# Performance work log

Hardware: AMD Instinct MI355X
Metric: run time of the kernel (lower is better)

Reference implementation:

```python
import jax, jax.numpy as jnp
import numpy as np

NODE = 5
FML = 64                     # hidden_size // node_num = 320 // 5
F0, F1, FO = 256, 256, 256   # fc_numbers
D_IN = (FML + 1) * 2         # each node has in-degree 2 -> 130
# graph[i,j]==1 means edge i->j; parents of node i = sorted nonzero of column i
# graph = ring: graph[i][(i+1)%5] = graph[i][(i+2)%5] = 1
PARENTS = np.array([[3, 4], [0, 4], [0, 1], [1, 2], [2, 3]], dtype=np.int32)
BN_EPS = 1e-5


def setup_inputs() -> dict:
    key = jax.random.key(0)
    ks = jax.random.split(key, 14)
    B, T = 8192, 128
    s = 0.05
    f32 = jnp.float32
    return {
        "x":   jax.random.normal(ks[0], (B, 1, NODE, T), f32),
        # stacked per-node MLP params (all 5 nodes share in-degree 2 -> same shapes)
        "W1":  (jax.random.normal(ks[1], (NODE, D_IN, F0), f32) * s),
        "b1":  jnp.zeros((NODE, F0), f32),
        "W2":  (jax.random.normal(ks[2], (NODE, F0, F1), f32) * s),
        "b2":  jnp.zeros((NODE, F1), f32),
        "W3":  (jax.random.normal(ks[3], (NODE, F1, FML), f32) * s),
        "b3":  jnp.zeros((NODE, FML), f32),
        # output head: (FML+1)*5 = 325 -> FO -> BN -> 7 -> softmax
        "Wo1": (jax.random.normal(ks[4], ((FML + 1) * NODE, FO), f32) * s),
        "bo1": jnp.zeros((FO,), f32),
        "gamma": jnp.ones((FO,), f32),
        "beta":  jnp.zeros((FO,), f32),
        "Wo2": (jax.random.normal(ks[5], (FO, 7), f32) * s),
        "bo2": jnp.zeros((7,), f32),
    }


def reference(x, W1, b1, W2, b2, W3, b3, Wo1, bo1, gamma, beta, Wo2, bo2):
    B, T = x.shape[0], x.shape[3]
    xs = x.reshape(B, NODE, T).transpose(2, 0, 1)  # [T, B, N]
    parents = jnp.asarray(PARENTS)                 # [N, 2]

    def step(state, x_t):
        # gather per-node parent observations and parent states
        xg = x_t[:, parents]                                   # [B, N, 2]
        sg = state[:, parents, :].reshape(B, NODE, 2 * FML)    # [B, N, 128]
        inp = jnp.concatenate([xg, sg], axis=-1)               # [B, N, 130]
        h = jax.nn.relu(jnp.einsum('bni,nio->bno', inp, W1) + b1)
        h = jax.nn.relu(jnp.einsum('bni,nio->bno', h, W2) + b2)
        new_state = jnp.tanh(jnp.einsum('bni,nio->bno', h, W3) + b3)  # [B, N, FML]
        return new_state, None

    state0 = jnp.zeros((B, NODE, FML), x.dtype)
    state, _ = jax.lax.scan(jax.checkpoint(step), state0, xs)

    feat = jnp.concatenate([xs[-1], state.reshape(B, -1)], axis=1)  # [B, 325]
    h = jax.nn.relu(feat @ Wo1 + bo1)                               # [B, FO]
    # BatchNorm1d in training mode: batch statistics (biased variance)
    mu = h.mean(axis=0)
    var = ((h - mu) ** 2).mean(axis=0)
    h = (h - mu) / jnp.sqrt(var + BN_EPS) * gamma + beta
    return jax.nn.softmax(h @ Wo2 + bo2, axis=1)                    # [B, 7]
```

## Files before the change

kernel.cpp:

```cpp
#include <hip/hip_runtime.h>
#include <cstddef>
#include <cstdint>

typedef _Float16 half8  __attribute__((ext_vector_type(8)));
typedef _Float16 half4v __attribute__((ext_vector_type(4)));
typedef float    floatx4 __attribute__((ext_vector_type(4)));
typedef unsigned long long u64;

#define NB 51
#define SW(row) (((row)&7)*8)

#define AGENT_LD(p)    __hip_atomic_load((p), __ATOMIC_RELAXED, __HIP_MEMORY_SCOPE_AGENT)
#define AGENT_ST(p,v)  __hip_atomic_store((p), (v), __ATOMIC_RELAXED, __HIP_MEMORY_SCOPE_AGENT)

#define HPRE_OFF 0u
#define SUM_OFF  8388608u
#define FLAG_OFF 8390656u
#define CONS_OFF 8391680u
#define SG_OFF   8392704u
#define PACK_OFF 18878464u
#define W1P_HALFS 163840
#define W2P_HALFS 327680
#define W3P_HALFS 81920
#define WS_NEEDED 20189184u

#define SMEM_BYTES 116352

__global__ __launch_bounds__(256) void pack_kernel(
    const float* __restrict__ W1, const float* __restrict__ W2,
    const float* __restrict__ W3, const float* __restrict__ Wo1,
    _Float16* __restrict__ w1p, _Float16* __restrict__ w2p,
    _Float16* __restrict__ w3p, _Float16* __restrict__ wo1p,
    float* __restrict__ sums, int* __restrict__ flags, int* __restrict__ cons)
{
    int id = blockIdx.x * 256 + threadIdx.x;
    if (id < 512) sums[id] = 0.f;
    if (id < 256) { flags[id] = 0; cons[id] = 0; }
    int f = id >> 6;
    int lane = id & 63;
    int q = lane >> 4, cl = lane & 15;
    if (f < 320) {
        int kk = f & 3, mt = (f >> 2) & 15, n = f >> 6;
        #pragma unroll
        for (int j = 0; j < 8; j++)
            w1p[(size_t)f*512 + lane*8 + j] =
                (_Float16)W1[(size_t)(n*130 + 2 + kk*32 + q*8 + j)*256 + mt*16 + cl];
    } else if (f < 960) {
        int g = f - 320;
        int kk = g & 7, mt = (g >> 3) & 15, n = g >> 7;
        #pragma unroll
        for (int j = 0; j < 8; j++)
            w2p[(size_t)g*512 + lane*8 + j] =
                (_Float16)W2[(size_t)(n*256 + kk*32 + q*8 + j)*256 + mt*16 + cl];
    } else if (f < 1120) {
        int g = f - 960;
        int kk = g & 7, mt = (g >> 3) & 3, n = g >> 5;
        #pragma unroll
        for (int j = 0; j < 8; j++)
            w3p[(size_t)g*512 + lane*8 + j] =
                (_Float16)W3[(size_t)(n*256 + kk*32 + q*8 + j)*64 + mt*16 + cl];
    } else if (f < 1280) {
        int g = f - 1120;
        int kk = g % 10, mt = g / 10;
        #pragma unroll
        for (int j = 0; j < 8; j++)
            wo1p[(size_t)g*512 + lane*8 + j] =
                (_Float16)Wo1[(size_t)(5 + kk*32 + q*8 + j)*256 + mt*16 + cl];
    }
}

template<int NT>
__device__ __attribute__((always_inline)) void scan_impl(
    const float* __restrict__ x, const float* __restrict__ W1,
    const float* __restrict__ b1, const float* __restrict__ b2, const float* __restrict__ b3,
    const _Float16* __restrict__ w1p, const _Float16* __restrict__ w2p,
    const _Float16* __restrict__ w3p,
    _Float16* __restrict__ Sg, int* flags, int* cons,
    char* smem, int n, int idx, int r0)
{
    constexpr int BB  = NT * 16;
    constexpr int NCH = 3;
    _Float16* Sp  = (_Float16*)smem;
    _Float16* H1  = (_Float16*)(smem + 45056);
    _Float16* H2  = (_Float16*)(smem + 77824);
    float*    xls = (float*)(smem + 110592);
    float*    cns = (float*)(smem + 112000);

    const int tid = threadIdx.x, w = tid >> 6, lane = tid & 63;
    const int quad = lane >> 4, cl = lane & 15;
    const int P0t[5] = {3,0,0,1,2}, P1t[5] = {4,4,1,2,3};
    const int p0 = P0t[n], p1 = P1t[n];
    const int myix = n*NB + idx, f0ix = p0*NB + idx, f1ix = p1*NB + idx;
    const int mt3 = w & 3, half = w >> 2;

    half8 w1f[2][4], w2f[2][8], w3f[8];
    #pragma unroll
    for (int i = 0; i < 2; i++) {
        int mt = 2*w + i;
        #pragma unroll
        for (int kk = 0; kk < 4; kk++)
            w1f[i][kk] = *(const half8*)(w1p + (size_t)((n*16 + mt)*4 + kk)*512 + lane*8);
        #pragma unroll
        for (int kk = 0; kk < 8; kk++)
            w2f[i][kk] = *(const half8*)(w2p + (size_t)((n*16 + mt)*8 + kk)*512 + lane*8);
    }
    #pragma unroll
    for (int kk = 0; kk < 8; kk++)
        w3f[kk] = *(const half8*)(w3p + (size_t)((n*4 + mt3)*8 + kk)*512 + lane*8);

    for (int i = tid; i < 1088; i += 512) {
        float v;
        if      (i < 256) v = b1[n*256 + i];
        else if (i < 512) v = b2[n*256 + i - 256];
        else if (i < 576) v = b3[n*64  + i - 512];
        else { int j = i - 576; v = W1[(size_t)(n*130 + (j>>8))*256 + (j & 255)]; }
        cns[i] = v;
    }

    auto stage_rows = [&](int first_row, int R, int buf) {
        int tot = 2*R*8;
        for (int i = tid; i < tot; i += 512) {
            int pp = i >= R*8;
            int rem = i - pp*R*8;
            int rl = rem >> 3, g8 = rem & 7;
            int grow = first_row + rl;
            u64* src = (u64*)(Sg + ((size_t)((buf*5 + (pp ? p1 : p0))*8192 + r0 + grow))*64 + g8*8);
            u64 lo = AGENT_LD(src);
            u64 hi = AGENT_LD(src + 1);
            union { u64 q[2]; half8 h; } u; u.q[0] = lo; u.q[1] = hi;
            *(half8*)&Sp[pp*11264 + grow*64 + ((g8*8) ^ SW(grow))] = u.h;
        }
    };

    for (int t = 0; t < 128; t++) {
        if (t > 0 && tid < 2) {
            int* fp = &flags[tid ? f1ix : f0ix];
            while (AGENT_LD(fp) < t) __builtin_amdgcn_s_sleep(2);
        }
        if (t >= 2 && tid == 2) {
            int need = 2*(t-1);
            while (AGENT_LD(&cons[myix]) < need) __builtin_amdgcn_s_sleep(2);
        }
        __syncthreads();

        if (t > 0) stage_rows(0, 64, (t-1) & 1);
        for (int i = tid; i < 2*BB; i += 512) {
            int pp = i >= BB; int rl = i - pp*BB;
            xls[pp*176 + rl] = x[(size_t)(r0 + rl)*640 + (pp ? p1 : p0)*128 + t];
        }
        __syncthreads();

        #pragma unroll
        for (int c = 0; c < NCH; c++) {
            const int rem_nt = NT - c*4;
            const int cnt = rem_nt < 4 ? rem_nt : 4;
            const int base16 = c*64;

            if (t > 0 && c + 1 < NCH) {
                int fr = (c+1)*64;
                int R = BB - fr; if (R > 64) R = 64;
                stage_rows(fr, R, (t-1) & 1);
            }

            floatx4 a1[2][4];
            #pragma unroll
            for (int i = 0; i < 2; i++) {
                int fb = (2*w + i)*16 + quad*4;
                floatx4 bv = *(const floatx4*)&cns[fb];
                floatx4 u0 = *(const floatx4*)&cns[576 + fb];
                floatx4 u1 = *(const floatx4*)&cns[832 + fb];
                #pragma unroll
                for (int j = 0; j < 4; j++) if (j < cnt) {
                    int rb = base16 + j*16 + cl;
                    float xa = xls[rb], xc = xls[176 + rb];
                    a1[i][j] = bv + u0*xa + u1*xc;
                }
            }
            if (t > 0) {
                #pragma unroll
                for (int kk = 0; kk < 4; kk++)
                    #pragma unroll
                    for (int j = 0; j < 4; j++) if (j < cnt) {
                        half8 bf = *(const half8*)&Sp[(kk>>1)*11264 + (base16 + j*16 + cl)*64
                                                      + (((kk&1)*32 + quad*8) ^ SW(cl))];
                        a1[0][j] = __builtin_amdgcn_mfma_f32_16x16x32_f16(w1f[0][kk], bf, a1[0][j], 0,0,0);
                        a1[1][j] = __builtin_amdgcn_mfma_f32_16x16x32_f16(w1f[1][kk], bf, a1[1][j], 0,0,0);
                    }
            }
            #pragma unroll
            for (int i = 0; i < 2; i++) {
                int fb = (2*w + i)*16 + quad*4;
                #pragma unroll
                for (int j = 0; j < 4; j++) if (j < cnt) {
                    int rl = j*16 + cl;
                    half4v pk;
                    #pragma unroll
                    for (int r = 0; r < 4; r++) {
                        float v = a1[i][j][r]; v = v > 0.f ? v : 0.f;
                        pk[r] = (_Float16)v;
                    }
                    *(half4v*)&H1[rl*256 + (fb ^ SW(cl))] = pk;
                }
            }
            __syncthreads();

            if (c == NCH-2 && t > 0 && tid < 2)
                __hip_atomic_fetch_add(&cons[tid ? f1ix : f0ix], 1,
                                       __ATOMIC_RELAXED, __HIP_MEMORY_SCOPE_AGENT);

            floatx4 a2[2][4];
            #pragma unroll
            for (int i = 0; i < 2; i++) {
                int fb = (2*w + i)*16 + quad*4;
                floatx4 bv = *(const floatx4*)&cns[256 + fb];
                #pragma unroll
                for (int j = 0; j < 4; j++) if (j < cnt) a2[i][j] = bv;
            }
            #pragma unroll
            for (int kk = 0; kk < 8; kk++)
                #pragma unroll
                for (int j = 0; j < 4; j++) if (j < cnt) {
                    half8 bf = *(const half8*)&H1[(j*16 + cl)*256 + ((kk*32 + quad*8) ^ SW(cl))];
                    a2[0][j] = __builtin_amdgcn_mfma_f32_16x16x32_f16(w2f[0][kk], bf, a2[0][j], 0,0,0);
                    a2[1][j] = __builtin_amdgcn_mfma_f32_16x16x32_f16(w2f[1][kk], bf, a2[1][j], 0,0,0);
                }
            #pragma unroll
            for (int i = 0; i < 2; i++) {
                int fb = (2*w + i)*16 + quad*4;
                #pragma unroll
                for (int j = 0; j < 4; j++) if (j < cnt) {
                    int rl = j*16 + cl;
                    half4v pk;
                    #pragma unroll
                    for (int r = 0; r < 4; r++) {
                        float v = a2[i][j][r]; v = v > 0.f ? v : 0.f;
                        pk[r] = (_Float16)v;
                    }
                    *(half4v*)&H2[rl*256 + (fb ^ SW(cl))] = pk;
                }
            }
            __syncthreads();

            {
                int f3 = mt3*16 + quad*4;
                floatx4 bv = *(const floatx4*)&cns[512 + f3];
                floatx4 a3[2];
                #pragma unroll
                for (int jj = 0; jj < 2; jj++) a3[jj] = bv;
                #pragma unroll
                for (int kk = 0; kk < 8; kk++)
                    #pragma unroll
                    for (int jj = 0; jj < 2; jj++) {
                        int j = half*2 + jj;
                        if (j < cnt) {
                            half8 bf = *(const half8*)&H2[(j*16 + cl)*256 + ((kk*32 + quad*8) ^ SW(cl))];
                            a3[jj] = __builtin_amdgcn_mfma_f32_16x16x32_f16(w3f[kk], bf, a3[jj], 0,0,0);
                        }
                    }
                #pragma unroll
                for (int jj = 0; jj < 2; jj++) {
                    int j = half*2 + jj;
                    if (j < cnt) {
                        int grow = r0 + base16 + j*16 + cl;
                        union { _Float16 hh[4]; u64 q; } pk;
                        #pragma unroll
                        for (int r = 0; r < 4; r++) pk.hh[r] = (_Float16)tanhf(a3[jj][r]);
                        AGENT_ST((u64*)(Sg + ((size_t)(((t&1)*5 + n)*8192 + grow))*64 + f3), pk.q);
                    }
                }
            }
        }

        __syncthreads();
        if (tid == 0)
            AGENT_ST(&flags[myix], t+1);
    }
}

__global__ __launch_bounds__(512, 2) void scan_kernel(
    const float* __restrict__ x, const float* __restrict__ W1,
    const float* __restrict__ b1, const float* __restrict__ b2, const float* __restrict__ b3,
    const _Float16* __restrict__ w1p, const _Float16* __restrict__ w2p,
    const _Float16* __restrict__ w3p,
    _Float16* __restrict__ Sg, int* flags, int* cons)
{
    extern __shared__ char smem[];
    int b = blockIdx.x;
    int n = b / NB, idx = b % NB;
    int r0 = idx < 2 ? idx*176 : 352 + (idx-2)*160;
    if (idx < 2)
        scan_impl<11>(x, W1, b1, b2, b3, w1p, w2p, w3p, Sg, flags, cons, smem, n, idx, r0);
    else
        scan_impl<10>(x, W1, b1, b2, b3, w1p, w2p, w3p, Sg, flags, cons, smem, n, idx, r0);
}

__global__ __launch_bounds__(512) void hpre_kernel(
    const float* __restrict__ x, const float* __restrict__ Wo1, const float* __restrict__ bo1,
    const _Float16* __restrict__ wo1p, const _Float16* __restrict__ Sg,
    float* __restrict__ hpre)
{
    __shared__ float x5[640];
    __shared__ float wxo[1280];
    __shared__ float bo1c[256];
    int tid = threadIdx.x, w = tid >> 6, lane = tid & 63;
    int quad = lane >> 4, cl = lane & 15;
    int r0h = blockIdx.x * 128;

    for (int i = tid; i < 640; i += 512)
        x5[i] = x[(size_t)(r0h + (i & 127))*640 + (i >> 7)*128 + 127];
    for (int i = tid; i < 1280; i += 512) wxo[i] = Wo1[i];
    if (tid < 256) bo1c[tid] = bo1[tid];

    half8 of[2][10];
    #pragma unroll
    for (int i = 0; i < 2; i++) {
        int mt = 2*w + i;
        #pragma unroll
        for (int kk = 0; kk < 10; kk++)
            of[i][kk] = *(const half8*)(wo1p + (size_t)(mt*10 + kk)*512 + lane*8);
    }
    __syncthreads();

    floatx4 acc[2][8];
    #pragma unroll
    for (int i = 0; i < 2; i++) {
        int fb = (2*w + i)*16 + quad*4;
        floatx4 bv = *(const floatx4*)&bo1c[fb];
        #pragma unroll
        for (int nt = 0; nt < 8; nt++) {
            floatx4 a = bv;
            #pragma unroll
            for (int p = 0; p < 5; p++) {
                floatx4 wv = *(const floatx4*)&wxo[p*256 + fb];
                float xv = x5[p*128 + nt*16 + cl];
                a += wv * xv;
            }
            acc[i][nt] = a;
        }
    }
    #pragma unroll
    for (int kk = 0; kk < 10; kk++) {
        int nd = kk >> 1;
        #pragma unroll
        for (int nt = 0; nt < 8; nt++) {
            const _Float16* sp = Sg + ((size_t)((5 + nd)*8192 + r0h + nt*16 + cl))*64
                                    + (kk & 1)*32 + quad*8;
            half8 bf = *(const half8*)sp;
            acc[0][nt] = __builtin_amdgcn_mfma_f32_16x16x32_f16(of[0][kk], bf, acc[0][nt], 0,0,0);
            acc[1][nt] = __builtin_amdgcn_mfma_f32_16x16x32_f16(of[1][kk], bf, acc[1][nt], 0,0,0);
        }
    }
    #pragma unroll
    for (int i = 0; i < 2; i++) {
        int fb = (2*w + i)*16 + quad*4;
        #pragma unroll
        for (int nt = 0; nt < 8; nt++) {
            floatx4 v = acc[i][nt];
            #pragma unroll
            for (int r = 0; r < 4; r++) v[r] = v[r] > 0.f ? v[r] : 0.f;
            *(floatx4*)&hpre[(size_t)(r0h + nt*16 + cl)*256 + fb] = v;
        }
    }
}

__global__ __launch_bounds__(256) void bnstats_kernel(const float* __restrict__ hpre,
                                                      float* __restrict__ sums)
{
    int col = threadIdx.x;
    int r0 = blockIdx.x * 128;
    float s = 0.f, s2 = 0.f;
    for (int r = 0; r < 128; r++) {
        float v = hpre[(size_t)(r0 + r)*256 + col];
        s += v; s2 += v*v;
    }
    atomicAdd(&sums[col], s);
    atomicAdd(&sums[256 + col], s2);
}

__global__ __launch_bounds__(256) void head_kernel(
    const float* __restrict__ hpre, const float* __restrict__ sums,
    const float* __restrict__ gamma, const float* __restrict__ beta,
    const float* __restrict__ Wo2, const float* __restrict__ bo2,
    float* __restrict__ out)
{
    int row  = blockIdx.x * 4 + (threadIdx.x >> 6);
    int lane = threadIdx.x & 63;
    floatx4 h  = *(const floatx4*)&hpre[(size_t)row*256 + lane*4];
    floatx4 sm = *(const floatx4*)&sums[lane*4];
    floatx4 sq = *(const floatx4*)&sums[256 + lane*4];
    floatx4 g  = *(const floatx4*)&gamma[lane*4];
    floatx4 bb = *(const floatx4*)&beta[lane*4];
    float acc[7] = {0.f,0.f,0.f,0.f,0.f,0.f,0.f};
    #pragma unroll
    for (int e = 0; e < 4; e++) {
        float mu  = sm[e] * (1.f/8192.f);
        float var = sq[e] * (1.f/8192.f) - mu*mu;
        float hn  = (h[e] - mu) * rsqrtf(var + 1e-5f) * g[e] + bb[e];
        int colg = lane*4 + e;
        #pragma unroll
        for (int j = 0; j < 7; j++) acc[j] += hn * Wo2[colg*7 + j];
    }
    #pragma unroll
    for (int off = 1; off < 64; off <<= 1) {
        #pragma unroll
        for (int j = 0; j < 7; j++) acc[j] += __shfl_xor(acc[j], off, 64);
    }
    float z[7], m = -1e30f;
    #pragma unroll
    for (int j = 0; j < 7; j++) { z[j] = acc[j] + bo2[j]; m = fmaxf(m, z[j]); }
    float se = 0.f;
    #pragma unroll
    for (int j = 0; j < 7; j++) { z[j] = expf(z[j] - m); se += z[j]; }
    if (lane < 7) out[(size_t)row*7 + lane] = z[lane] / se;
}

extern "C" void kernel_launch(void* const* d_in, const int* in_sizes, int n_in,
                              void* d_out, int out_size, void* d_ws, size_t ws_size,
                              hipStream_t stream)
{
    const float* x    = (const float*)d_in[0];
    const float* W1   = (const float*)d_in[1];
    const float* b1   = (const float*)d_in[2];
    const float* W2   = (const float*)d_in[3];
    const float* b2   = (const float*)d_in[4];
    const float* W3   = (const float*)d_in[5];
    const float* b3   = (const float*)d_in[6];
    const float* Wo1  = (const float*)d_in[7];
    const float* bo1  = (const float*)d_in[8];
    const float* gamma= (const float*)d_in[9];
    const float* beta = (const float*)d_in[10];
    const float* Wo2  = (const float*)d_in[11];
    const float* bo2  = (const float*)d_in[12];
    float* out = (float*)d_out;

    if (ws_size < WS_NEEDED) return;
    char* ws = (char*)d_ws;
    float*     hpre  = (float*)(ws + HPRE_OFF);
    float*     sums  = (float*)(ws + SUM_OFF);
    int*       flags = (int*)(ws + FLAG_OFF);
    int*       cons  = (int*)(ws + CONS_OFF);
    _Float16*  Sg    = (_Float16*)(ws + SG_OFF);
    _Float16*  w1p   = (_Float16*)(ws + PACK_OFF);
    _Float16*  w2p   = w1p + W1P_HALFS;
    _Float16*  w3p   = w2p + W2P_HALFS;
    _Float16*  wo1p  = w3p + W3P_HALFS;

    hipFuncSetAttribute((const void*)scan_kernel,
                        hipFuncAttributeMaxDynamicSharedMemorySize, SMEM_BYTES);

    pack_kernel<<<320, 256, 0, stream>>>(W1, W2, W3, Wo1, w1p, w2p, w3p, wo1p,
                                         sums, flags, cons);
    scan_kernel<<<5*NB, 512, SMEM_BYTES, stream>>>(x, W1, b1, b2, b3,
                                                   w1p, w2p, w3p, Sg, flags, cons);
    hpre_kernel<<<64, 512, 0, stream>>>(x, Wo1, bo1, wo1p, Sg, hpre);
    bnstats_kernel<<<64, 256, 0, stream>>>(hpre, sums);
    head_kernel<<<2048, 256, 0, stream>>>(hpre, sums, gamma, beta, Wo2, bo2, out);
}
```

Before: 2.053 ms.

## Retile layer-2 MFMA work across waves and use exp2-based tanh

Layer 2 is repartitioned so each wave computes 4 output M-tiles over 2 row tiles instead of 2 M-tiles over 4 row tiles. Each H1 fragment read from LDS is then reused across four MFMAs, which halves the shared-memory reads per wave, at the cost of holding twice as many W2 fragments in registers. The tanh for the recurrent state is replaced with a clamped exp2-based formula to cut transcendental cost, and the ReLU selects become fmaxf. The larger register footprint may lower occupancy or cause spills under the 512x2 launch bounds.

```diff
diff --git a/kernel.cpp b/kernel.cpp
--- a/kernel.cpp
+++ b/kernel.cpp
@@ -26,6 +26,12 @@
 
 #define SMEM_BYTES 116352
 
+__device__ __forceinline__ float fast_tanh(float v) {
+    v = fminf(fmaxf(v, -15.f), 15.f);
+    float a = exp2f(v * 2.88539008177793f);
+    return (a - 1.f) / (a + 1.f);
+}
+
 __global__ __launch_bounds__(256) void pack_kernel(
     const float* __restrict__ W1, const float* __restrict__ W2,
     const float* __restrict__ W3, const float* __restrict__ Wo1,
@@ -92,14 +98,19 @@
     const int p0 = P0t[n], p1 = P1t[n];
     const int myix = n*NB + idx, f0ix = p0*NB + idx, f1ix = p1*NB + idx;
     const int mt3 = w & 3, half = w >> 2;
-
-    half8 w1f[2][4], w2f[2][8], w3f[8];
+    const int mtg = w & 3, rh = w >> 2;
+
+    half8 w1f[2][4], w2f[4][8], w3f[8];
     #pragma unroll
     for (int i = 0; i < 2; i++) {
         int mt = 2*w + i;
         #pragma unroll
         for (int kk = 0; kk < 4; kk++)
             w1f[i][kk] = *(const half8*)(w1p + (size_t)((n*16 + mt)*4 + kk)*512 + lane*8);
+    }
+    #pragma unroll
+    for (int i = 0; i < 4; i++) {
+        int mt = mtg*4 + i;
         #pragma unroll
         for (int kk = 0; kk < 8; kk++)
             w2f[i][kk] = *(const half8*)(w2p + (size_t)((n*16 + mt)*8 + kk)*512 + lane*8);
@@ -162,44 +173,44 @@
                 stage_rows(fr, R, (t-1) & 1);
             }
 
-            floatx4 a1[2][4];
-            #pragma unroll
-            for (int i = 0; i < 2; i++) {
-                int fb = (2*w + i)*16 + quad*4;
-                floatx4 bv = *(const floatx4*)&cns[fb];
-                floatx4 u0 = *(const floatx4*)&cns[576 + fb];
-                floatx4 u1 = *(const floatx4*)&cns[832 + fb];
-                #pragma unroll
-                for (int j = 0; j < 4; j++) if (j < cnt) {
-                    int rb = base16 + j*16 + cl;
-                    float xa = xls[rb], xc = xls[176 + rb];
-                    a1[i][j] = bv + u0*xa + u1*xc;
-                }
-            }
-            if (t > 0) {
-                #pragma unroll
-                for (int kk = 0; kk < 4; kk++)
+            {
+                floatx4 a1[2][4];
+                #pragma unroll
+                for (int i = 0; i < 2; i++) {
+                    int fb = (2*w + i)*16 + quad*4;
+                    floatx4 bv = *(const floatx4*)&cns[fb];
+                    floatx4 u0 = *(const floatx4*)&cns[576 + fb];
+                    floatx4 u1 = *(const floatx4*)&cns[832 + fb];
                     #pragma unroll
                     for (int j = 0; j < 4; j++) if (j < cnt) {
-                        half8 bf = *(const half8*)&Sp[(kk>>1)*11264 + (base16 + j*16 + cl)*64
-                                                      + (((kk&1)*32 + quad*8) ^ SW(cl))];
-                        a1[0][j] = __builtin_amdgcn_mfma_f32_16x16x32_f16(w1f[0][kk], bf, a1[0][j], 0,0,0);
-                        a1[1][j] = __builtin_amdgcn_mfma_f32_16x16x32_f16(w1f[1][kk], bf, a1[1][j], 0,0,0);
-                    }
-            }
-            #pragma unroll
-            for (int i = 0; i < 2; i++) {
-                int fb = (2*w + i)*16 + quad*4;
-                #pragma unroll
-                for (int j = 0; j < 4; j++) if (j < cnt) {
-                    int rl = j*16 + cl;
-                    half4v pk;
-                    #pragma unroll
-                    for (int r = 0; r < 4; r++) {
-                        float v = a1[i][j][r]; v = v > 0.f ? v : 0.f;
-                        pk[r] = (_Float16)v;
-                    }
-                    *(half4v*)&H1[rl*256 + (fb ^ SW(cl))] = pk;
+                        int rb = base16 + j*16 + cl;
+                        float xa = xls[rb], xc = xls[176 + rb];
+                        a1[i][j] = bv + u0*xa + u1*xc;
+                    }
+                }
+                if (t > 0) {
+                    #pragma unroll
+                    for (int kk = 0; kk < 4; kk++)
+                        #pragma unroll
+                        for (int j = 0; j < 4; j++) if (j < cnt) {
+                            half8 bf = *(const half8*)&Sp[(kk>>1)*11264 + (base16 + j*16 + cl)*64
+                                                          + (((kk&1)*32 + quad*8) ^ SW(cl))];
+                            a1[0][j] = __builtin_amdgcn_mfma_f32_16x16x32_f16(w1f[0][kk], bf, a1[0][j], 0,0,0);
+                            a1[1][j] = __builtin_amdgcn_mfma_f32_16x16x32_f16(w1f[1][kk], bf, a1[1][j], 0,0,0);
+                        }
+                }
+                #pragma unroll
+                for (int i = 0; i < 2; i++) {
+                    int fb = (2*w + i)*16 + quad*4;
+                    #pragma unroll
+                    for (int j = 0; j < 4; j++) if (j < cnt) {
+                        int rl = j*16 + cl;
+                        half4v pk;
+                        #pragma unroll
+                        for (int r = 0; r < 4; r++)
+                            pk[r] = (_Float16)fmaxf(a1[i][j][r], 0.f);
+                        *(half4v*)&H1[rl*256 + (fb ^ SW(cl))] = pk;
+                    }
                 }
             }
             __syncthreads();
@@ -208,35 +219,42 @@
                 __hip_atomic_fetch_add(&cons[tid ? f1ix : f0ix], 1,
                                        __ATOMIC_RELAXED, __HIP_MEMORY_SCOPE_AGENT);
 
-            floatx4 a2[2][4];
-            #pragma unroll
-            for (int i = 0; i < 2; i++) {
-                int fb = (2*w + i)*16 + quad*4;
-                floatx4 bv = *(const floatx4*)&cns[256 + fb];
-                #pragma unroll
-                for (int j = 0; j < 4; j++) if (j < cnt) a2[i][j] = bv;
-            }
-            #pragma unroll
-            for (int kk = 0; kk < 8; kk++)
-                #pragma unroll
-                for (int j = 0; j < 4; j++) if (j < cnt) {
-                    half8 bf = *(const half8*)&H1[(j*16 + cl)*256 + ((kk*32 + quad*8) ^ SW(cl))];
-                    a2[0][j] = __builtin_amdgcn_mfma_f32_16x16x32_f16(w2f[0][kk], bf, a2[0][j], 0,0,0);
-                    a2[1][j] = __builtin_amdgcn_mfma_f32_16x16x32_f16(w2f[1][kk], bf, a2[1][j], 0,0,0);
-                }
-            #pragma unroll
-            for (int i = 0; i < 2; i++) {
-                int fb = (2*w + i)*16 + quad*4;
-                #pragma unroll
-                for (int j = 0; j < 4; j++) if (j < cnt) {
-                    int rl = j*16 + cl;
-                    half4v pk;
-                    #pragma unroll
-                    for (int r = 0; r < 4; r++) {
-                        float v = a2[i][j][r]; v = v > 0.f ? v : 0.f;
-                        pk[r] = (_Float16)v;
-                    }
-                    *(half4v*)&H2[rl*256 + (fb ^ SW(cl))] = pk;
+            {
+                floatx4 a2[4][2];
+                #pragma unroll
+                for (int i = 0; i < 4; i++) {
+                    int fb = (mtg*4 + i)*16 + quad*4;
+                    floatx4 bv = *(const floatx4*)&cns[256 + fb];
+                    #pragma unroll
+                    for (int jj = 0; jj < 2; jj++) a2[i][jj] = bv;
+                }
+                #pragma unroll
+                for (int kk = 0; kk < 8; kk++)
+                    #pragma unroll
+                    for (int jj = 0; jj < 2; jj++) {
+                        int j = rh*2 + jj;
+                        if (j < cnt) {
+                            half8 bf = *(const half8*)&H1[(j*16 + cl)*256 + ((kk*32 + quad*8) ^ SW(cl))];
+                            #pragma unroll
+                            for (int i = 0; i < 4; i++)
+                                a2[i][jj] = __builtin_amdgcn_mfma_f32_16x16x32_f16(w2f[i][kk], bf, a2[i][jj], 0,0,0);
+                        }
+                    }
+                #pragma unroll
+                for (int i = 0; i < 4; i++) {
+                    int fb = (mtg*4 + i)*16 + quad*4;
+                    #pragma unroll
+                    for (int jj = 0; jj < 2; jj++) {
+                        int j = rh*2 + jj;
+                        if (j < cnt) {
+                            int rl = j*16 + cl;
+                            half4v pk;
+                            #pragma unroll
+                            for (int r = 0; r < 4; r++)
+                                pk[r] = (_Float16)fmaxf(a2[i][jj][r], 0.f);
+                            *(half4v*)&H2[rl*256 + (fb ^ SW(cl))] = pk;
+                        }
+                    }
                 }
             }
             __syncthreads();
@@ -264,7 +282,7 @@
                         int grow = r0 + base16 + j*16 + cl;
                         union { _Float16 hh[4]; u64 q; } pk;
                         #pragma unroll
-                        for (int r = 0; r < 4; r++) pk.hh[r] = (_Float16)tanhf(a3[jj][r]);
+                        for (int r = 0; r < 4; r++) pk.hh[r] = (_Float16)fast_tanh(a3[jj][r]);
                         AGENT_ST((u64*)(Sg + ((size_t)(((t&1)*5 + n)*8192 + grow))*64 + f3), pk.q);
                     }
                 }
@@ -357,7 +375,7 @@
         for (int nt = 0; nt < 8; nt++) {
             floatx4 v = acc[i][nt];
             #pragma unroll
-            for (int r = 0; r < 4; r++) v[r] = v[r] > 0.f ? v[r] : 0.f;
+            for (int r = 0; r < 4; r++) v[r] = fmaxf(v[r], 0.f);
             *(floatx4*)&hpre[(size_t)(r0h + nt*16 + cl)*256 + fb] = v;
         }
     }
```

Result: slower. 3.099 ms (+51.0%).

## Stage parent states via async global-to-LDS DMA, double-buffer x, use fast tanh

Applied to the files above, without the earlier changes.

Parent-state rows are now staged into LDS by a single wavefront using global_load_lds DMA, with the XOR swizzle applied on the source side, replacing the per-thread agent loads and LDS stores. Flag polling and the first staging chunk also move to that wavefront. The x column for step t+1 is prefetched into a double-buffered LDS slot during the last chunk, and the consumer-count increment moves to the final chunk. tanhf is replaced by an exp2-based approximation, and relu selects become fmaxf. This trades fewer instructions on the serial per-step path for a DMA ordering and visibility risk, since the staged rows are read after only a __syncthreads, and for slightly lower tanh accuracy.

```diff
diff --git a/kernel.cpp b/kernel.cpp
--- a/kernel.cpp
+++ b/kernel.cpp
@@ -12,6 +12,11 @@
 
 #define AGENT_LD(p)    __hip_atomic_load((p), __ATOMIC_RELAXED, __HIP_MEMORY_SCOPE_AGENT)
 #define AGENT_ST(p,v)  __hip_atomic_store((p), (v), __ATOMIC_RELAXED, __HIP_MEMORY_SCOPE_AGENT)
+
+typedef __attribute__((address_space(3))) void lds_vt;
+typedef const __attribute__((address_space(1))) void gbl_vt;
+#define DMA16_SC1(src, dst) \
+    __builtin_amdgcn_global_load_lds((gbl_vt*)(src), (lds_vt*)(dst), 16, 0, 16)
 
 #define HPRE_OFF 0u
 #define SUM_OFF  8388608u
@@ -24,7 +29,13 @@
 #define W3P_HALFS 81920
 #define WS_NEEDED 20189184u
 
-#define SMEM_BYTES 116352
+#define SMEM_BYTES 117760
+
+__device__ __forceinline__ float fast_tanh(float v) {
+    v = fminf(fmaxf(v, -15.f), 15.f);
+    float a = exp2f(v * 2.88539008177793f);
+    return (a - 1.f) / (a + 1.f);
+}
 
 __global__ __launch_bounds__(256) void pack_kernel(
     const float* __restrict__ W1, const float* __restrict__ W2,
@@ -84,7 +95,7 @@
     _Float16* H1  = (_Float16*)(smem + 45056);
     _Float16* H2  = (_Float16*)(smem + 77824);
     float*    xls = (float*)(smem + 110592);
-    float*    cns = (float*)(smem + 112000);
+    float*    cns = (float*)(smem + 113408);
 
     const int tid = threadIdx.x, w = tid >> 6, lane = tid & 63;
     const int quad = lane >> 4, cl = lane & 15;
@@ -116,37 +127,36 @@
         else { int j = i - 576; v = W1[(size_t)(n*130 + (j>>8))*256 + (j & 255)]; }
         cns[i] = v;
     }
-
-    auto stage_rows = [&](int first_row, int R, int buf) {
-        int tot = 2*R*8;
-        for (int i = tid; i < tot; i += 512) {
-            int pp = i >= R*8;
-            int rem = i - pp*R*8;
-            int rl = rem >> 3, g8 = rem & 7;
-            int grow = first_row + rl;
-            u64* src = (u64*)(Sg + ((size_t)((buf*5 + (pp ? p1 : p0))*8192 + r0 + grow))*64 + g8*8);
-            u64 lo = AGENT_LD(src);
-            u64 hi = AGENT_LD(src + 1);
-            union { u64 q[2]; half8 h; } u; u.q[0] = lo; u.q[1] = hi;
-            *(half8*)&Sp[pp*11264 + grow*64 + ((g8*8) ^ SW(grow))] = u.h;
+    for (int i = tid; i < 2*BB; i += 512) {
+        int pp = i >= BB; int rl = i - pp*BB;
+        xls[pp*176 + rl] = x[(size_t)(r0 + rl)*640 + (pp ? p1 : p0)*128 + 0];
+    }
+
+    auto stage_dma = [&](int first_row, int R, int buf) {
+        int groups = R >> 3;
+        for (int q = 0; q < 2*groups; q++) {
+            int pp  = q >= groups;
+            int grp = q - pp*groups;
+            int rl  = first_row + grp*8 + (lane >> 3);
+            int g8  = (lane & 7) ^ (rl & 7);
+            const _Float16* src = Sg
+                + ((size_t)((buf*5 + (pp ? p1 : p0))*8192 + r0 + rl))*64 + g8*8;
+            DMA16_SC1(src, &Sp[pp*11264 + (first_row + grp*8)*64]);
         }
     };
 
     for (int t = 0; t < 128; t++) {
-        if (t > 0 && tid < 2) {
-            int* fp = &flags[tid ? f1ix : f0ix];
-            while (AGENT_LD(fp) < t) __builtin_amdgcn_s_sleep(2);
-        }
-        if (t >= 2 && tid == 2) {
-            int need = 2*(t-1);
-            while (AGENT_LD(&cons[myix]) < need) __builtin_amdgcn_s_sleep(2);
-        }
-        __syncthreads();
-
-        if (t > 0) stage_rows(0, 64, (t-1) & 1);
-        for (int i = tid; i < 2*BB; i += 512) {
-            int pp = i >= BB; int rl = i - pp*BB;
-            xls[pp*176 + rl] = x[(size_t)(r0 + rl)*640 + (pp ? p1 : p0)*128 + t];
+        const int xb = (t & 1) * 352;
+        if (w == 0) {
+            if (t > 0 && lane < 2) {
+                int* fp = &flags[lane ? f1ix : f0ix];
+                while (AGENT_LD(fp) < t) __builtin_amdgcn_s_sleep(1);
+            }
+            if (t >= 2 && lane == 2) {
+                int need = 2*(t-1);
+                while (AGENT_LD(&cons[myix]) < need) __builtin_amdgcn_s_sleep(1);
+            }
+            if (t > 0) stage_dma(0, 64, (t-1) & 1);
         }
         __syncthreads();
 
@@ -156,87 +166,95 @@
             const int cnt = rem_nt < 4 ? rem_nt : 4;
             const int base16 = c*64;
 
-            if (t > 0 && c + 1 < NCH) {
-                int fr = (c+1)*64;
-                int R = BB - fr; if (R > 64) R = 64;
-                stage_rows(fr, R, (t-1) & 1);
-            }
-
-            floatx4 a1[2][4];
-            #pragma unroll
-            for (int i = 0; i < 2; i++) {
-                int fb = (2*w + i)*16 + quad*4;
-                floatx4 bv = *(const floatx4*)&cns[fb];
-                floatx4 u0 = *(const floatx4*)&cns[576 + fb];
-                floatx4 u1 = *(const floatx4*)&cns[832 + fb];
-                #pragma unroll
-                for (int j = 0; j < 4; j++) if (j < cnt) {
-                    int rb = base16 + j*16 + cl;
-                    float xa = xls[rb], xc = xls[176 + rb];
-                    a1[i][j] = bv + u0*xa + u1*xc;
-                }
-            }
-            if (t > 0) {
-                #pragma unroll
-                for (int kk = 0; kk < 4; kk++)
+            if (c + 1 < NCH) {
+                if (w == 0 && t > 0) {
+                    int fr = (c+1)*64;
+                    int R = BB - fr; if (R > 64) R = 64;
+                    stage_dma(fr, R, (t-1) & 1);
+                }
+            } else if (t < 127) {
+                for (int i = tid; i < 2*BB; i += 512) {
+                    int pp = i >= BB; int rl = i - pp*BB;
+                    xls[((t+1)&1)*352 + pp*176 + rl] =
+                        x[(size_t)(r0 + rl)*640 + (pp ? p1 : p0)*128 + (t+1)];
+                }
+            }
+
+            {
+                floatx4 a1[2][4];
+                #pragma unroll
+                for (int i = 0; i < 2; i++) {
+                    int fb = (2*w + i)*16 + quad*4;
+                    floatx4 bv = *(const floatx4*)&cns[fb];
+                    floatx4 u0 = *(const floatx4*)&cns[576 + fb];
+                    floatx4 u1 = *(const floatx4*)&cns[832 + fb];
                     #pragma unroll
                     for (int j = 0; j < 4; j++) if (j < cnt) {
-                        half8 bf = *(const half8*)&Sp[(kk>>1)*11264 + (base16 + j*16 + cl)*64
-                                                      + (((kk&1)*32 + quad*8) ^ SW(cl))];
-                        a1[0][j] = __builtin_amdgcn_mfma_f32_16x16x32_f16(w1f[0][kk], bf, a1[0][j], 0,0,0);
-                        a1[1][j] = __builtin_amdgcn_mfma_f32_16x16x32_f16(w1f[1][kk], bf, a1[1][j], 0,0,0);
-                    }
-            }
-            #pragma unroll
-            for (int i = 0; i < 2; i++) {
-                int fb = (2*w + i)*16 + quad*4;
-                #pragma unroll
-                for (int j = 0; j < 4; j++) if (j < cnt) {
-                    int rl = j*16 + cl;
-                    half4v pk;
-                    #pragma unroll
-                    for (int r = 0; r < 4; r++) {
-                        float v = a1[i][j][r]; v = v > 0.f ? v : 0.f;
-                        pk[r] = (_Float16)v;
-                    }
-                    *(half4v*)&H1[rl*256 + (fb ^ SW(cl))] = pk;
+                        int rb = base16 + j*16 + cl;
+                        float xa = xls[xb + rb], xc = xls[xb + 176 + rb];
+                        a1[i][j] = bv + u0*xa + u1*xc;
+                    }
+                }
+                if (t > 0) {
+                    #pragma unroll
+                    for (int kk = 0; kk < 4; kk++)
+                        #pragma unroll
+                        for (int j = 0; j < 4; j++) if (j < cnt) {
+                            half8 bf = *(const half8*)&Sp[(kk>>1)*11264 + (base16 + j*16 + cl)*64
+                                                          + (((kk&1)*32 + quad*8) ^ SW(cl))];
+                            a1[0][j] = __builtin_amdgcn_mfma_f32_16x16x32_f16(w1f[0][kk], bf, a1[0][j], 0,0,0);
+                            a1[1][j] = __builtin_amdgcn_mfma_f32_16x16x32_f16(w1f[1][kk], bf, a1[1][j], 0,0,0);
+                        }
+                }
+                #pragma unroll
+                for (int i = 0; i < 2; i++) {
+                    int fb = (2*w + i)*16 + quad*4;
+                    #pragma unroll
+                    for (int j = 0; j < 4; j++) if (j < cnt) {
+                        int rl = j*16 + cl;
+                        half4v pk;
+                        #pragma unroll
+                        for (int r = 0; r < 4; r++)
+                            pk[r] = (_Float16)fmaxf(a1[i][j][r], 0.f);
+                        *(half4v*)&H1[rl*256 + (fb ^ SW(cl))] = pk;
+                    }
                 }
             }
             __syncthreads();
 
-            if (c == NCH-2 && t > 0 && tid < 2)
+            if (c == NCH-1 && t > 0 && tid < 2)
                 __hip_atomic_fetch_add(&cons[tid ? f1ix : f0ix], 1,
                                        __ATOMIC_RELAXED, __HIP_MEMORY_SCOPE_AGENT);
 
-            floatx4 a2[2][4];
-            #pragma unroll
-            for (int i = 0; i < 2; i++) {
-                int fb = (2*w + i)*16 + quad*4;
-                floatx4 bv = *(const floatx4*)&cns[256 + fb];
-                #pragma unroll
-                for (int j = 0; j < 4; j++) if (j < cnt) a2[i][j] = bv;
-            }
-            #pragma unroll
-            for (int kk = 0; kk < 8; kk++)
-                #pragma unroll
-                for (int j = 0; j < 4; j++) if (j < cnt) {
-                    half8 bf = *(const half8*)&H1[(j*16 + cl)*256 + ((kk*32 + quad*8) ^ SW(cl))];
-                    a2[0][j] = __builtin_amdgcn_mfma_f32_16x16x32_f16(w2f[0][kk], bf, a2[0][j], 0,0,0);
-                    a2[1][j] = __builtin_amdgcn_mfma_f32_16x16x32_f16(w2f[1][kk], bf, a2[1][j], 0,0,0);
-                }
-            #pragma unroll
-            for (int i = 0; i < 2; i++) {
-                int fb = (2*w + i)*16 + quad*4;
-                #pragma unroll
-                for (int j = 0; j < 4; j++) if (j < cnt) {
-                    int rl = j*16 + cl;
-                    half4v pk;
-                    #pragma unroll
-                    for (int r = 0; r < 4; r++) {
-                        float v = a2[i][j][r]; v = v > 0.f ? v : 0.f;
-                        pk[r] = (_Float16)v;
-                    }
-                    *(half4v*)&H2[rl*256 + (fb ^ SW(cl))] = pk;
+            {
+                floatx4 a2[2][4];
+                #pragma unroll
+                for (int i = 0; i < 2; i++) {
+                    int fb = (2*w + i)*16 + quad*4;
+                    floatx4 bv = *(const floatx4*)&cns[256 + fb];
+                    #pragma unroll
+                    for (int j = 0; j < 4; j++) if (j < cnt) a2[i][j] = bv;
+                }
+                #pragma unroll
+                for (int kk = 0; kk < 8; kk++)
+                    #pragma unroll
+                    for (int j = 0; j < 4; j++) if (j < cnt) {
+                        half8 bf = *(const half8*)&H1[(j*16 + cl)*256 + ((kk*32 + quad*8) ^ SW(cl))];
+                        a2[0][j] = __builtin_amdgcn_mfma_f32_16x16x32_f16(w2f[0][kk], bf, a2[0][j], 0,0,0);
+                        a2[1][j] = __builtin_amdgcn_mfma_f32_16x16x32_f16(w2f[1][kk], bf, a2[1][j], 0,0,0);
+                    }
+                #pragma unroll
+                for (int i = 0; i < 2; i++) {
+                    int fb = (2*w + i)*16 + quad*4;
+                    #pragma unroll
+                    for (int j = 0; j < 4; j++) if (j < cnt) {
+                        int rl = j*16 + cl;
+                        half4v pk;
+                        #pragma unroll
+                        for (int r = 0; r < 4; r++)
+                            pk[r] = (_Float16)fmaxf(a2[i][j][r], 0.f);
+                        *(half4v*)&H2[rl*256 + (fb ^ SW(cl))] = pk;
+                    }
                 }
             }
             __syncthreads();
@@ -264,7 +282,7 @@
                         int grow = r0 + base16 + j*16 + cl;
                         union { _Float16 hh[4]; u64 q; } pk;
                         #pragma unroll
-                        for (int r = 0; r < 4; r++) pk.hh[r] = (_Float16)tanhf(a3[jj][r]);
+                        for (int r = 0; r < 4; r++) pk.hh[r] = (_Float16)fast_tanh(a3[jj][r]);
                         AGENT_ST((u64*)(Sg + ((size_t)(((t&1)*5 + n)*8192 + grow))*64 + f3), pk.q);
                     }
                 }
@@ -357,7 +375,7 @@
         for (int nt = 0; nt < 8; nt++) {
             floatx4 v = acc[i][nt];
             #pragma unroll
-            for (int r = 0; r < 4; r++) v[r] = v[r] > 0.f ? v[r] : 0.f;
+            for (int r = 0; r < 4; r++) v[r] = fmaxf(v[r], 0.f);
             *(floatx4*)&hpre[(size_t)(r0h + nt*16 + cl)*256 + fb] = v;
         }
     }
```

New measurement: 1.858 ms. 9.5% less time.
